# Performance work log

Measured on AMD Instinct MI355X. Metric: run time of the kernel, lower is better.

Reference implementation:

```python
import jax, jax.numpy as jnp
import numpy as np

D = 512
H = 8
FFN_H = 2048
NEG = -1.0e10


def layer_norm(x, gamma, beta, eps=1e-5):
    mu = jnp.mean(x, axis=-1, keepdims=True)
    var = jnp.var(x, axis=-1, keepdims=True)
    return (x - mu) * jax.lax.rsqrt(var + eps) * gamma + beta


def mha(x_q, x_kv, Wq, Wk, Wv, Wo, valid_lens):
    # x_q: [B,Tq,D], x_kv: [B,Tk,D]; valid_lens: [B,Tq] or [B]
    B, Tq, _ = x_q.shape
    Tk = x_kv.shape[1]
    dh = D // H
    q = (x_q @ Wq.T).reshape(B, Tq, H, dh).transpose(0, 2, 1, 3)  # [B,H,Tq,dh]
    k = (x_kv @ Wk.T).reshape(B, Tk, H, dh).transpose(0, 2, 1, 3)
    v = (x_kv @ Wv.T).reshape(B, Tk, H, dh).transpose(0, 2, 1, 3)
    scores = jnp.einsum('bhqd,bhkd->bhqk', q, k) / jnp.sqrt(jnp.float32(dh))
    pos = jnp.arange(Tk)
    if valid_lens.ndim == 1:  # [B] -> mask [B,1,1,Tk]
        mask = pos[None, None, None, :] < valid_lens[:, None, None, None]
    else:  # [B,Tq] -> mask [B,1,Tq,Tk]
        mask = pos[None, None, None, :] < valid_lens[:, None, :, None]
    scores = jnp.where(mask, scores, NEG)
    attn = jax.nn.softmax(scores, axis=-1)
    out = jnp.einsum('bhqk,bhkd->bhqd', attn, v)  # [B,H,Tq,dh]
    out = out.transpose(0, 2, 1, 3).reshape(B, Tq, D)
    return out @ Wo.T


def setup_inputs() -> dict:
    key = jax.random.key(0)
    ks = jax.random.split(key, 20)
    B, T = 32, 512
    s = 1.0 / np.sqrt(D)
    inp = {
        'X': jax.random.normal(ks[0], (B, T, D), jnp.float32),
        'enc_outputs': jax.random.normal(ks[1], (B, T, D), jnp.float32),
        'dec_valid_lens': jax.random.randint(ks[2], (B, T), 1, T + 1, jnp.int32),
        'enc_valid_lens': jax.random.randint(ks[3], (B,), 1, T + 1, jnp.int32),
    }
    names = ['Wq1', 'Wk1', 'Wv1', 'Wo1', 'Wq2', 'Wk2', 'Wv2', 'Wo2']
    for i, n in enumerate(names):
        inp[n] = jax.random.normal(ks[4 + i], (D, D), jnp.float32) * s
    inp['W1'] = jax.random.normal(ks[12], (FFN_H, D), jnp.float32) * s
    inp['b1'] = jnp.zeros((FFN_H,), jnp.float32)
    inp['W2'] = jax.random.normal(ks[13], (D, FFN_H), jnp.float32) * (1.0 / np.sqrt(FFN_H))
    inp['b2'] = jnp.zeros((D,), jnp.float32)
    for j in (1, 2, 3):
        inp[f'g{j}'] = jnp.ones((D,), jnp.float32)
        inp[f'be{j}'] = jnp.zeros((D,), jnp.float32)
    return inp


def reference(X, enc_outputs, dec_valid_lens, enc_valid_lens,
              Wq1, Wk1, Wv1, Wo1, Wq2, Wk2, Wv2, Wo2,
              W1, b1, W2, b2, g1, be1, g2, be2, g3, be3):
    # Training path: state[2][i] is None -> key_values = X. Dropout in eval mode (identity).
    X2 = mha(X, X, Wq1, Wk1, Wv1, Wo1, dec_valid_lens)            # self-attention
    Y = layer_norm(X + X2, g1, be1)                               # AddNorm1
    Y2 = mha(Y, enc_outputs, Wq2, Wk2, Wv2, Wo2, enc_valid_lens)  # cross-attention
    Z = layer_norm(Y + Y2, g2, be2)                               # AddNorm2
    F = (jax.nn.leaky_relu(Z @ W1.T + b1, 0.01)) @ W2.T + b2      # FFN (LeakyReLU slope 0.01)
    return layer_norm(Z + F, g3, be3)                             # AddNorm3
```

## Files before the change

### kernel.cpp

```cpp
#include <hip/hip_runtime.h>
#include <cstdint>
#include <cstddef>

typedef __bf16 bf16;
typedef __bf16 bf16x8 __attribute__((ext_vector_type(8)));
typedef float  f32x4  __attribute__((ext_vector_type(4)));
typedef unsigned short u16;

#define MD ((size_t)8388608)

__device__ __forceinline__ void async_copy16(const bf16* gp, bf16* lp) {
  __builtin_amdgcn_global_load_lds(
      (__attribute__((address_space(1))) void*)(gp),
      (__attribute__((address_space(3))) void*)(lp), 16, 0, 0);
}

__device__ __forceinline__ int is_f32(const u16* __restrict__ x) {
  const int e = (x[(threadIdx.x & 63) * 2] >> 7) & 0xFF;
  return __ballot(e >= 141) != 0ull;
}

struct ConvSrc { const void* p[20]; };

__global__ __launch_bounds__(256)
void convert_all(ConvSrc s, bf16* __restrict__ ws, const u16* __restrict__ xprobe)
{
  const int n[20] = {8388608, 8388608,
                     262144, 262144, 262144, 262144, 262144, 262144, 262144, 262144,
                     1048576, 2048, 1048576, 512, 512, 512, 512, 512, 512, 512};
  const unsigned int doff[20] = {
      41943040u, 50331648u,
      58720256u, 58982400u, 59244544u, 59506688u,
      59768832u, 60030976u, 60293120u, 60555264u,
      60817408u, 61865984u, 61868032u, 62916608u,
      62917120u, 62917632u, 62918144u, 62918656u, 62919168u, 62919680u};

  const int f32 = is_f32(xprobe);

  int bi = blockIdx.x;
  int idx = 0, b0 = 0;
  for (; idx < 20; ++idx) {
    const int nb = (n[idx] + 2047) >> 11;
    if (bi < b0 + nb) break;
    b0 += nb;
  }
  const int i = ((bi - b0) << 11) + threadIdx.x * 8;
  if (i >= n[idx]) return;
  bf16* dst = ws + doff[idx] + i;
  if (f32) {
    const float* sp = (const float*)s.p[idx] + i;
    f32x4 a = *(const f32x4*)sp;
    f32x4 b = *(const f32x4*)(sp + 4);
    bf16x8 o;
#pragma unroll
    for (int e = 0; e < 4; ++e) { o[e] = (bf16)a[e]; o[4 + e] = (bf16)b[e]; }
    *(bf16x8*)dst = o;
  } else {
    *(bf16x8*)dst = *(const bf16x8*)((const bf16*)s.p[idx] + i);
  }
}

template<int MODE, int TM, int TN>
__global__ __launch_bounds__(256)
void gemm_bt(const bf16* __restrict__ A, const bf16* __restrict__ B,
             const bf16* __restrict__ bias, bf16* __restrict__ C,
             int M, int N, int K)
{
  constexpr int MI = TM / 32;
  constexpr int NJ = TN / 32;
  __shared__ __attribute__((aligned(16))) bf16 As[TM * 64];
  __shared__ __attribute__((aligned(16))) bf16 Bs[TN * 64];

  const int t    = threadIdx.x;
  const int wave = t >> 6;
  const int lane = t & 63;
  const int quad = lane >> 4;
  const int l15  = lane & 15;
  const int wr   = (wave >> 1) * (TM / 2);
  const int wc   = (wave & 1) * (TN / 2);

  const int id    = blockIdx.y * gridDim.x + blockIdx.x;
  const int chunk = (gridDim.x * gridDim.y) >> 3;
  const int lin   = (id & 7) * chunk + (id >> 3);
  const int m0    = (lin / gridDim.x) * TM;
  const int n0    = (lin % gridDim.x) * TN;

  const f32x4 fz = {0.f, 0.f, 0.f, 0.f};
  f32x4 acc[MI][NJ];
#pragma unroll
  for (int i = 0; i < MI; ++i)
#pragma unroll
    for (int j = 0; j < NJ; ++j) acc[i][j] = fz;

  const int nkt = K >> 6;
  for (int kt = 0; kt < nkt; ++kt) {
    const int k0 = kt << 6;
    __syncthreads();
#pragma unroll
    for (int c = 0; c < TM / 32; ++c) {
      const int s   = c * 256 + t;
      const int row = s >> 3;
      const int kg  = ((s & 7) ^ (row & 7)) << 3;
      async_copy16(A + (size_t)(m0 + row) * K + k0 + kg,
                   As + ((c * 256 + wave * 64) << 3));
    }
#pragma unroll
    for (int c = 0; c < TN / 32; ++c) {
      const int s   = c * 256 + t;
      const int row = s >> 3;
      const int kg  = ((s & 7) ^ (row & 7)) << 3;
      async_copy16(B + (size_t)(n0 + row) * K + k0 + kg,
                   Bs + ((c * 256 + wave * 64) << 3));
    }
    __syncthreads();

#pragma unroll
    for (int ks = 0; ks < 2; ++ks) {
      bf16x8 af[MI], bfv[NJ];
#pragma unroll
      for (int i = 0; i < MI; ++i) {
        const int row = wr + i * 16 + l15;
        const int ph  = (ks * 4 + quad) ^ (row & 7);
        af[i] = *(const bf16x8*)(As + row * 64 + ph * 8);
      }
#pragma unroll
      for (int j = 0; j < NJ; ++j) {
        const int row = wc + j * 16 + l15;
        const int ph  = (ks * 4 + quad) ^ (row & 7);
        bfv[j] = *(const bf16x8*)(Bs + row * 64 + ph * 8);
      }
#pragma unroll
      for (int i = 0; i < MI; ++i)
#pragma unroll
        for (int j = 0; j < NJ; ++j)
          acc[i][j] = __builtin_amdgcn_mfma_f32_16x16x32_bf16(af[i], bfv[j],
                                                              acc[i][j], 0, 0, 0);
    }
  }

#pragma unroll
  for (int i = 0; i < MI; ++i) {
    const int m = m0 + wr + i * 16 + quad * 4;
#pragma unroll
    for (int j = 0; j < NJ; ++j) {
      const int n = n0 + wc + j * 16 + l15;
      float bv = 0.f;
      if (MODE >= 1) bv = (float)bias[n];
#pragma unroll
      for (int r = 0; r < 4; ++r) {
        float v = acc[i][j][r];
        if (MODE >= 1) v += bv;
        if (MODE == 1) v = v > 0.f ? v : 0.01f * v;
        C[(size_t)(m + r) * N + n] = (bf16)v;
      }
    }
  }
}

__global__ __launch_bounds__(256, 4)
void flash_attn(const bf16* __restrict__ Qp, const bf16* __restrict__ Kp,
                const bf16* __restrict__ Vp, bf16* __restrict__ Op,
                const int* __restrict__ vlen, int per_query, int sq, int skv)
{
  __shared__ __attribute__((aligned(16))) bf16 Ks[64][72];
  __shared__ __attribute__((aligned(16))) bf16 VsT[64][72];
  __shared__ __attribute__((aligned(16))) bf16 Ps[4][32][72];
  __shared__ int vlmax_sh;

  const int t    = threadIdx.x;
  const int wave = t >> 6;
  const int lane = t & 63;
  const int quad = lane >> 4;
  const int l15  = lane & 15;
  const int bx   = blockIdx.x;
  const int qt   = bx >> 8;
  const int h    = bx & 7;
  const int b    = (bx >> 3) & 31;
  const int q0   = qt * 128 + wave * 32;

  bf16x8 qfrag[2][2];
#pragma unroll
  for (int mt = 0; mt < 2; ++mt)
#pragma unroll
    for (int ks = 0; ks < 2; ++ks)
      qfrag[mt][ks] = *(const bf16x8*)(Qp +
          (size_t)(b * 512 + q0 + mt * 16 + l15) * sq + h * 64 + ks * 32 + quad * 8);

  int vl_r[2][4];
  int myvl = 1;
#pragma unroll
  for (int mt = 0; mt < 2; ++mt)
#pragma unroll
    for (int r = 0; r < 4; ++r) {
      const int q = q0 + mt * 16 + quad * 4 + r;
      const int v = per_query ? vlen[b * 512 + q] : vlen[b];
      vl_r[mt][r] = v;
      myvl = v > myvl ? v : myvl;
    }

  if (t == 0) vlmax_sh = 1;
  __syncthreads();
#pragma unroll
  for (int off = 1; off < 64; off <<= 1) {
    const int o = __shfl_xor(myvl, off);
    myvl = o > myvl ? o : myvl;
  }
  if (lane == 0) atomicMax(&vlmax_sh, myvl);
  __syncthreads();
  const int ktiles = (vlmax_sh + 63) >> 6;

  const f32x4 fz = {0.f, 0.f, 0.f, 0.f};
  float l_part[2][4] = {{0.f,0.f,0.f,0.f},{0.f,0.f,0.f,0.f}};
  f32x4 o_acc[2][4];
#pragma unroll
  for (int mt = 0; mt < 2; ++mt)
#pragma unroll
    for (int nt = 0; nt < 4; ++nt) o_acc[mt][nt] = fz;

  for (int kt = 0; kt < ktiles; ++kt) {
    const int k0 = kt * 64;
    __syncthreads();
    {
      const int r0 = t >> 3;
      const int c0 = (t & 7) * 8;
      const bf16* g = Kp + (size_t)(b * 512 + k0 + r0) * skv + h * 64 + c0;
      *(bf16x8*)&Ks[r0][c0]      = *(const bf16x8*)g;
      *(bf16x8*)&Ks[r0 + 32][c0] = *(const bf16x8*)(g + (size_t)32 * skv);
    }
    {
      const bf16* g = Vp + (size_t)(b * 512 + k0 + wave * 16) * skv + h * 64 + lane;
      bf16x8 lo, hi;
#pragma unroll
      for (int kk = 0; kk < 8; ++kk) lo[kk] = g[(size_t)kk * skv];
#pragma unroll
      for (int kk = 0; kk < 8; ++kk) hi[kk] = g[(size_t)(kk + 8) * skv];
      *(bf16x8*)&VsT[lane][wave * 16]     = lo;
      *(bf16x8*)&VsT[lane][wave * 16 + 8] = hi;
    }
    __syncthreads();

    f32x4 s[2][4];
#pragma unroll
    for (int mt = 0; mt < 2; ++mt)
#pragma unroll
      for (int nt = 0; nt < 4; ++nt) s[mt][nt] = fz;
#pragma unroll
    for (int ks = 0; ks < 2; ++ks)
#pragma unroll
      for (int nt = 0; nt < 4; ++nt) {
        const bf16x8 bk = *(const bf16x8*)&Ks[nt * 16 + l15][ks * 32 + quad * 8];
        s[0][nt] = __builtin_amdgcn_mfma_f32_16x16x32_bf16(qfrag[0][ks], bk, s[0][nt], 0, 0, 0);
        s[1][nt] = __builtin_amdgcn_mfma_f32_16x16x32_bf16(qfrag[1][ks], bk, s[1][nt], 0, 0, 0);
      }

#pragma unroll
    for (int mt = 0; mt < 2; ++mt)
#pragma unroll
      for (int nt = 0; nt < 4; ++nt) {
        const int k_abs = k0 + nt * 16 + l15;
#pragma unroll
        for (int r = 0; r < 4; ++r) {
          const float p = (k_abs < vl_r[mt][r]) ? __expf(s[mt][nt][r] * 0.125f) : 0.f;
          l_part[mt][r] += p;
          Ps[wave][mt * 16 + quad * 4 + r][nt * 16 + l15] = (bf16)p;
        }
      }

#pragma unroll
    for (int ks = 0; ks < 2; ++ks) {
      const bf16x8 ap0 = *(const bf16x8*)&Ps[wave][l15][ks * 32 + quad * 8];
      const bf16x8 ap1 = *(const bf16x8*)&Ps[wave][16 + l15][ks * 32 + quad * 8];
#pragma unroll
      for (int nt = 0; nt < 4; ++nt) {
        const bf16x8 bv = *(const bf16x8*)&VsT[nt * 16 + l15][ks * 32 + quad * 8];
        o_acc[0][nt] = __builtin_amdgcn_mfma_f32_16x16x32_bf16(ap0, bv, o_acc[0][nt], 0, 0, 0);
        o_acc[1][nt] = __builtin_amdgcn_mfma_f32_16x16x32_bf16(ap1, bv, o_acc[1][nt], 0, 0, 0);
      }
    }
  }

#pragma unroll
  for (int mt = 0; mt < 2; ++mt)
#pragma unroll
    for (int r = 0; r < 4; ++r) {
      float l = l_part[mt][r];
#pragma unroll
      for (int off = 1; off < 16; off <<= 1)
        l += __shfl_xor(l, off);
      const float inv_l = (l > 0.f) ? (1.f / l) : 0.f;
      const int q = q0 + mt * 16 + quad * 4 + r;
#pragma unroll
      for (int nt = 0; nt < 4; ++nt)
        Op[(size_t)(b * 512 + q) * 512 + h * 64 + nt * 16 + l15] =
            (bf16)(o_acc[mt][nt][r] * inv_l);
    }
}

__global__ __launch_bounds__(256)
void add_layernorm(const bf16* X, const bf16* R,
                   const bf16* __restrict__ gamma, const bf16* __restrict__ beta,
                   bf16* Out)
{
  const int t    = threadIdx.x;
  const int wave = t >> 6;
  const int lane = t & 63;
  const size_t row  = (size_t)blockIdx.x * 4 + wave;
  const size_t base = row * 512 + lane * 8;

  bf16x8 xv = *(const bf16x8*)(X + base);
  bf16x8 rv = *(const bf16x8*)(R + base);
  float v[8];
  float sum = 0.f, ss = 0.f;
#pragma unroll
  for (int i = 0; i < 8; ++i) {
    v[i] = (float)xv[i] + (float)rv[i];
    sum += v[i];
    ss  += v[i] * v[i];
  }
#pragma unroll
  for (int off = 1; off < 64; off <<= 1) {
    sum += __shfl_xor(sum, off);
    ss  += __shfl_xor(ss, off);
  }
  const float mean = sum * (1.f / 512.f);
  const float var  = ss * (1.f / 512.f) - mean * mean;
  const float rstd = rsqrtf(var + 1e-5f);

  bf16x8 gv = *(const bf16x8*)(gamma + lane * 8);
  bf16x8 bv = *(const bf16x8*)(beta + lane * 8);
  bf16x8 ov;
#pragma unroll
  for (int i = 0; i < 8; ++i)
    ov[i] = (bf16)(((v[i] - mean) * rstd) * (float)gv[i] + (float)bv[i]);
  *(bf16x8*)(Out + base) = ov;
}

__global__ __launch_bounds__(256)
void add_layernorm_out(const bf16* X, const bf16* R,
                       const bf16* __restrict__ gamma, const bf16* __restrict__ beta,
                       void* Out, const u16* __restrict__ xprobe)
{
  const int t    = threadIdx.x;
  const int wave = t >> 6;
  const int lane = t & 63;
  const size_t row  = (size_t)blockIdx.x * 4 + wave;
  const size_t base = row * 512 + lane * 8;

  const int f32 = is_f32(xprobe);

  bf16x8 xv = *(const bf16x8*)(X + base);
  bf16x8 rv = *(const bf16x8*)(R + base);
  float v[8];
  float sum = 0.f, ss = 0.f;
#pragma unroll
  for (int i = 0; i < 8; ++i) {
    v[i] = (float)xv[i] + (float)rv[i];
    sum += v[i];
    ss  += v[i] * v[i];
  }
#pragma unroll
  for (int off = 1; off < 64; off <<= 1) {
    sum += __shfl_xor(sum, off);
    ss  += __shfl_xor(ss, off);
  }
  const float mean = sum * (1.f / 512.f);
  const float var  = ss * (1.f / 512.f) - mean * mean;
  const float rstd = rsqrtf(var + 1e-5f);

  bf16x8 gv = *(const bf16x8*)(gamma + lane * 8);
  bf16x8 bv = *(const bf16x8*)(beta + lane * 8);
  float o[8];
#pragma unroll
  for (int i = 0; i < 8; ++i)
    o[i] = ((v[i] - mean) * rstd) * (float)gv[i] + (float)bv[i];

  if (f32) {
    float* op = (float*)Out + base;
    f32x4 o0 = {o[0], o[1], o[2], o[3]};
    f32x4 o1 = {o[4], o[5], o[6], o[7]};
    *(f32x4*)op       = o0;
    *(f32x4*)(op + 4) = o1;
  } else {
    bf16x8 ov;
#pragma unroll
    for (int i = 0; i < 8; ++i) ov[i] = (bf16)o[i];
    *(bf16x8*)((bf16*)Out + base) = ov;
  }
}

extern "C" void kernel_launch(void* const* d_in, const int* in_sizes, int n_in,
                              void* d_out, int out_size, void* d_ws, size_t ws_size,
                              hipStream_t stream)
{
  (void)in_sizes; (void)n_in; (void)out_size; (void)ws_size;

  const int* dvl = (const int*)d_in[2];
  const int* evl = (const int*)d_in[3];
  const u16* xprobe = (const u16*)d_in[0];

  bf16* ws = (bf16*)d_ws;
  bf16* S0 = ws;
  bf16* S1 = ws + 1 * MD;
  bf16* S3 = ws + 3 * MD;
  bf16* S4 = ws + 4 * MD;
  bf16* Xb = ws + 5 * MD;
  bf16* Eb = ws + 6 * MD;
  bf16* W  = ws + 7 * MD;
  const bf16 *Wq1 = W,
             *Wo1 = W + 786432,   *Wq2 = W + 1048576, *Wk2 = W + 1310720,
             *Wo2 = W + 1835008,
             *W1  = W + 2097152,  *b1  = W + 3145728,
             *W2  = W + 3147776,  *b2  = W + 4196352,
             *g1  = W + 4196864,  *be1 = W + 4197376,
             *g2  = W + 4197888,  *be2 = W + 4198400,
             *g3  = W + 4198912,  *be3 = W + 4199424;

  ConvSrc cs;
  cs.p[0] = d_in[0];  cs.p[1] = d_in[1];
  for (int k = 0; k < 12; ++k) cs.p[2 + k] = d_in[4 + k];
  for (int k = 0; k < 6; ++k)  cs.p[14 + k] = d_in[16 + k];
  convert_all<<<dim3(10248), dim3(256), 0, stream>>>(cs, ws, xprobe);

  dim3 blk(256);
  dim3 gP(4, 128);
  dim3 gQKV(12, 128);
  dim3 gKV(8, 128);
  dim3 gF1(16, 128);

  gemm_bt<0,128,128><<<gQKV, blk, 0, stream>>>(Xb, Wq1, nullptr, S0, 16384, 1536, 512);
  flash_attn<<<dim3(1024), blk, 0, stream>>>(S0, S0 + 512, S0 + 1024, S3, dvl, 1, 1536, 1536);
  gemm_bt<0,128,128><<<gP, blk, 0, stream>>>(S3, Wo1, nullptr, S1, 16384, 512, 512);
  add_layernorm<<<dim3(4096), blk, 0, stream>>>(Xb, S1, g1, be1, S4);

  gemm_bt<0,128,128><<<gP,  blk, 0, stream>>>(S4, Wq2, nullptr, S0, 16384, 512, 512);
  gemm_bt<0,128,128><<<gKV, blk, 0, stream>>>(Eb, Wk2, nullptr, S1, 16384, 1024, 512);
  flash_attn<<<dim3(1024), blk, 0, stream>>>(S0, S1, S1 + 512, S3, evl, 0, 512, 1024);
  gemm_bt<0,128,128><<<gP, blk, 0, stream>>>(S3, Wo2, nullptr, S1, 16384, 512, 512);
  add_layernorm<<<dim3(4096), blk, 0, stream>>>(S4, S1, g2, be2, S4);

  gemm_bt<1,128,128><<<gF1, blk, 0, stream>>>(S4, W1, b1, S0, 16384, 2048, 512);
  gemm_bt<2,128,128><<<gP,  blk, 0, stream>>>(S0, W2, b2, Xb, 16384, 512, 2048);
  add_layernorm_out<<<dim3(4096), blk, 0, stream>>>(S4, Xb, g3, be3, d_out, xprobe);
}
```

Measured before the change: 473.2 us.

## Replace GEMM with double-buffered 8-wave 256-row tile kernel with ping-pong scheduling

Replaces the single-buffered 128x128 GEMM with a 512-thread kernel that uses 256-row tiles and double-buffered LDS for A and B. Loads for the next k-step are issued asynchronously while the current step's MFMAs run, and each step is split into two halves with barriers and raised wave priority around the MFMA bursts. The goal is to hide global-load latency and raise data reuse per block. In exchange it uses much more LDS and registers, and the hand-written vmcnt waits make correctness depend on the exact number of loads issued.

```diff
diff --git a/kernel.cpp b/kernel.cpp
--- a/kernel.cpp
+++ b/kernel.cpp
@@ -60,30 +60,54 @@
   }
 }
 
-template<int MODE, int TM, int TN>
-__global__ __launch_bounds__(256)
-void gemm_bt(const bf16* __restrict__ A, const bf16* __restrict__ B,
-             const bf16* __restrict__ bias, bf16* __restrict__ C,
-             int M, int N, int K)
-{
-  constexpr int MI = TM / 32;
-  constexpr int NJ = TN / 32;
-  __shared__ __attribute__((aligned(16))) bf16 As[TM * 64];
-  __shared__ __attribute__((aligned(16))) bf16 Bs[TN * 64];
+template<int ROWS>
+__device__ __forceinline__ void stage_tile(const bf16* __restrict__ g,
+                                           bf16* lds, int K)
+{
+  const int t = threadIdx.x;
+  const int wbase = (t >> 6) << 6;
+#pragma unroll
+  for (int r = 0; r < ROWS / 64; ++r) {
+    const int s   = (r << 9) + t;
+    const int row = s >> 3;
+    const int cg  = s & 7;
+    async_copy16(g + (size_t)row * K + ((cg ^ (row & 7)) << 3),
+                 lds + ((size_t)((r << 9) + wbase) << 3));
+  }
+}
+
+template<int MODE, int BN, int WM, int WN>
+__global__ __launch_bounds__(512, 2)
+void gemm8p(const bf16* __restrict__ A, const bf16* __restrict__ B,
+            const bf16* __restrict__ bias, bf16* __restrict__ C,
+            int M, int N, int K)
+{
+  constexpr int BM = 256;
+  constexpr int WR = BM / WM;
+  constexpr int MI = WR / 16;
+  constexpr int NJ = 4;
+  constexpr int MH = MI / 2;
+  constexpr int BL = BN / 64;
+
+  __shared__ __attribute__((aligned(16))) bf16 As[2][BM * 64];
+  __shared__ __attribute__((aligned(16))) bf16 Bs[2][BN * 64];
 
   const int t    = threadIdx.x;
-  const int wave = t >> 6;
   const int lane = t & 63;
   const int quad = lane >> 4;
   const int l15  = lane & 15;
-  const int wr   = (wave >> 1) * (TM / 2);
-  const int wc   = (wave & 1) * (TN / 2);
+  const int wave = t >> 6;
+  const int wm   = wave / WN;
+  const int wn   = wave % WN;
 
   const int id    = blockIdx.y * gridDim.x + blockIdx.x;
   const int chunk = (gridDim.x * gridDim.y) >> 3;
   const int lin   = (id & 7) * chunk + (id >> 3);
-  const int m0    = (lin / gridDim.x) * TM;
-  const int n0    = (lin % gridDim.x) * TN;
+  const int m0    = (lin / gridDim.x) * BM;
+  const int n0    = (lin % gridDim.x) * BN;
+
+  const bf16* Ag = A + (size_t)m0 * K;
+  const bf16* Bg = B + (size_t)n0 * K;
 
   const f32x4 fz = {0.f, 0.f, 0.f, 0.f};
   f32x4 acc[MI][NJ];
@@ -93,62 +117,97 @@
     for (int j = 0; j < NJ; ++j) acc[i][j] = fz;
 
   const int nkt = K >> 6;
+
+  stage_tile<BM>(Ag, As[0], K);
+  stage_tile<BN>(Bg, Bs[0], K);
+  stage_tile<BN>(Bg + (nkt > 1 ? 64 : 0), Bs[1], K);
+  if constexpr (BL == 4) asm volatile("s_waitcnt vmcnt(4)" ::: "memory");
+  else                   asm volatile("s_waitcnt vmcnt(2)" ::: "memory");
+  __builtin_amdgcn_s_barrier();
+
   for (int kt = 0; kt < nkt; ++kt) {
-    const int k0 = kt << 6;
-    __syncthreads();
-#pragma unroll
-    for (int c = 0; c < TM / 32; ++c) {
-      const int s   = c * 256 + t;
-      const int row = s >> 3;
-      const int kg  = ((s & 7) ^ (row & 7)) << 3;
-      async_copy16(A + (size_t)(m0 + row) * K + k0 + kg,
-                   As + ((c * 256 + wave * 64) << 3));
-    }
-#pragma unroll
-    for (int c = 0; c < TN / 32; ++c) {
-      const int s   = c * 256 + t;
-      const int row = s >> 3;
-      const int kg  = ((s & 7) ^ (row & 7)) << 3;
-      async_copy16(B + (size_t)(n0 + row) * K + k0 + kg,
-                   Bs + ((c * 256 + wave * 64) << 3));
-    }
-    __syncthreads();
-
-#pragma unroll
-    for (int ks = 0; ks < 2; ++ks) {
-      bf16x8 af[MI], bfv[NJ];
-#pragma unroll
-      for (int i = 0; i < MI; ++i) {
-        const int row = wr + i * 16 + l15;
-        const int ph  = (ks * 4 + quad) ^ (row & 7);
-        af[i] = *(const bf16x8*)(As + row * 64 + ph * 8);
-      }
-#pragma unroll
-      for (int j = 0; j < NJ; ++j) {
-        const int row = wc + j * 16 + l15;
-        const int ph  = (ks * 4 + quad) ^ (row & 7);
-        bfv[j] = *(const bf16x8*)(Bs + row * 64 + ph * 8);
-      }
-#pragma unroll
-      for (int i = 0; i < MI; ++i)
-#pragma unroll
-        for (int j = 0; j < NJ; ++j)
-          acc[i][j] = __builtin_amdgcn_mfma_f32_16x16x32_bf16(af[i], bfv[j],
-                                                              acc[i][j], 0, 0, 0);
-    }
-  }
-
-#pragma unroll
-  for (int i = 0; i < MI; ++i) {
-    const int m = m0 + wr + i * 16 + quad * 4;
-#pragma unroll
-    for (int j = 0; j < NJ; ++j) {
-      const int n = n0 + wc + j * 16 + l15;
+    const int c = kt & 1;
+    const bf16* a_l = As[c];
+    const bf16* b_l = Bs[c];
+    const int kA = (kt + 1 < nkt) ? kt + 1 : nkt - 1;
+    const int kB = (kt + 2 < nkt) ? kt + 2 : nkt - 1;
+
+    bf16x8 bfv[NJ][2];
+    bf16x8 af[MH][2];
+
+    stage_tile<BM>(Ag + ((size_t)kA << 6), As[c ^ 1], K);
+#pragma unroll
+    for (int nj = 0; nj < NJ; ++nj) {
+      const int row = wn * 64 + nj * 16 + l15;
+#pragma unroll
+      for (int ks = 0; ks < 2; ++ks) {
+        const int ph = (ks * 4 + quad) ^ (row & 7);
+        bfv[nj][ks] = *(const bf16x8*)(b_l + row * 64 + ph * 8);
+      }
+    }
+#pragma unroll
+    for (int mi = 0; mi < MH; ++mi) {
+      const int row = wm * WR + mi * 16 + l15;
+#pragma unroll
+      for (int ks = 0; ks < 2; ++ks) {
+        const int ph = (ks * 4 + quad) ^ (row & 7);
+        af[mi][ks] = *(const bf16x8*)(a_l + row * 64 + ph * 8);
+      }
+    }
+    __builtin_amdgcn_s_barrier();
+    asm volatile("s_waitcnt lgkmcnt(0)" ::: "memory");
+    __builtin_amdgcn_s_setprio(1);
+#pragma unroll
+    for (int mi = 0; mi < MH; ++mi)
+#pragma unroll
+      for (int nj = 0; nj < NJ; ++nj)
+#pragma unroll
+        for (int ks = 0; ks < 2; ++ks)
+          acc[mi][nj] = __builtin_amdgcn_mfma_f32_16x16x32_bf16(
+              af[mi][ks], bfv[nj][ks], acc[mi][nj], 0, 0, 0);
+    __builtin_amdgcn_s_setprio(0);
+    __builtin_amdgcn_s_barrier();
+
+    stage_tile<BN>(Bg + ((size_t)kB << 6), Bs[c], K);
+#pragma unroll
+    for (int mi = 0; mi < MH; ++mi) {
+      const int row = wm * WR + (MH + mi) * 16 + l15;
+#pragma unroll
+      for (int ks = 0; ks < 2; ++ks) {
+        const int ph = (ks * 4 + quad) ^ (row & 7);
+        af[mi][ks] = *(const bf16x8*)(a_l + row * 64 + ph * 8);
+      }
+    }
+    __builtin_amdgcn_s_barrier();
+    asm volatile("s_waitcnt lgkmcnt(0)" ::: "memory");
+    __builtin_amdgcn_s_setprio(1);
+#pragma unroll
+    for (int mi = 0; mi < MH; ++mi)
+#pragma unroll
+      for (int nj = 0; nj < NJ; ++nj)
+#pragma unroll
+        for (int ks = 0; ks < 2; ++ks)
+          acc[MH + mi][nj] = __builtin_amdgcn_mfma_f32_16x16x32_bf16(
+              af[mi][ks], bfv[nj][ks], acc[MH + mi][nj], 0, 0, 0);
+    __builtin_amdgcn_s_setprio(0);
+    if constexpr (BL == 4) asm volatile("s_waitcnt vmcnt(4)" ::: "memory");
+    else                   asm volatile("s_waitcnt vmcnt(2)" ::: "memory");
+    __builtin_amdgcn_s_barrier();
+  }
+
+  asm volatile("s_waitcnt vmcnt(0)" ::: "memory");
+
+#pragma unroll
+  for (int mi = 0; mi < MI; ++mi) {
+    const int m = m0 + wm * WR + mi * 16 + quad * 4;
+#pragma unroll
+    for (int nj = 0; nj < NJ; ++nj) {
+      const int n = n0 + wn * 64 + nj * 16 + l15;
       float bv = 0.f;
       if (MODE >= 1) bv = (float)bias[n];
 #pragma unroll
       for (int r = 0; r < 4; ++r) {
-        float v = acc[i][j][r];
+        float v = acc[mi][nj][r];
         if (MODE >= 1) v += bv;
         if (MODE == 1) v = v > 0.f ? v : 0.01f * v;
         C[(size_t)(m + r) * N + n] = (bf16)v;
@@ -421,24 +480,21 @@
   for (int k = 0; k < 6; ++k)  cs.p[14 + k] = d_in[16 + k];
   convert_all<<<dim3(10248), dim3(256), 0, stream>>>(cs, ws, xprobe);
 
-  dim3 blk(256);
-  dim3 gP(4, 128);
-  dim3 gQKV(12, 128);
-  dim3 gKV(8, 128);
-  dim3 gF1(16, 128);
-
-  gemm_bt<0,128,128><<<gQKV, blk, 0, stream>>>(Xb, Wq1, nullptr, S0, 16384, 1536, 512);
-  flash_attn<<<dim3(1024), blk, 0, stream>>>(S0, S0 + 512, S0 + 1024, S3, dvl, 1, 1536, 1536);
-  gemm_bt<0,128,128><<<gP, blk, 0, stream>>>(S3, Wo1, nullptr, S1, 16384, 512, 512);
-  add_layernorm<<<dim3(4096), blk, 0, stream>>>(Xb, S1, g1, be1, S4);
-
-  gemm_bt<0,128,128><<<gP,  blk, 0, stream>>>(S4, Wq2, nullptr, S0, 16384, 512, 512);
-  gemm_bt<0,128,128><<<gKV, blk, 0, stream>>>(Eb, Wk2, nullptr, S1, 16384, 1024, 512);
-  flash_attn<<<dim3(1024), blk, 0, stream>>>(S0, S1, S1 + 512, S3, evl, 0, 512, 1024);
-  gemm_bt<0,128,128><<<gP, blk, 0, stream>>>(S3, Wo2, nullptr, S1, 16384, 512, 512);
-  add_layernorm<<<dim3(4096), blk, 0, stream>>>(S4, S1, g2, be2, S4);
-
-  gemm_bt<1,128,128><<<gF1, blk, 0, stream>>>(S4, W1, b1, S0, 16384, 2048, 512);
-  gemm_bt<2,128,128><<<gP,  blk, 0, stream>>>(S0, W2, b2, Xb, 16384, 512, 2048);
-  add_layernorm_out<<<dim3(4096), blk, 0, stream>>>(S4, Xb, g3, be3, d_out, xprobe);
-}
+  dim3 blk256(256);
+  dim3 blk512(512);
+
+  gemm8p<0,256,2,4><<<dim3(6,64), blk512, 0, stream>>>(Xb, Wq1, nullptr, S0, 16384, 1536, 512);
+  flash_attn<<<dim3(1024), blk256, 0, stream>>>(S0, S0 + 512, S0 + 1024, S3, dvl, 1, 1536, 1536);
+  gemm8p<0,128,4,2><<<dim3(4,64), blk512, 0, stream>>>(S3, Wo1, nullptr, S1, 16384, 512, 512);
+  add_layernorm<<<dim3(4096), blk256, 0, stream>>>(Xb, S1, g1, be1, S4);
+
+  gemm8p<0,128,4,2><<<dim3(4,64), blk512, 0, stream>>>(S4, Wq2, nullptr, S0, 16384, 512, 512);
+  gemm8p<0,256,2,4><<<dim3(4,64), blk512, 0, stream>>>(Eb, Wk2, nullptr, S1, 16384, 1024, 512);
+  flash_attn<<<dim3(1024), blk256, 0, stream>>>(S0, S1, S1 + 512, S3, evl, 0, 512, 1024);
+  gemm8p<0,128,4,2><<<dim3(4,64), blk512, 0, stream>>>(S3, Wo2, nullptr, S1, 16384, 512, 512);
+  add_layernorm<<<dim3(4096), blk256, 0, stream>>>(S4, S1, g2, be2, S4);
+
+  gemm8p<1,256,2,4><<<dim3(8,64), blk512, 0, stream>>>(S4, W1, b1, S0, 16384, 2048, 512);
+  gemm8p<2,128,4,2><<<dim3(4,64), blk512, 0, stream>>>(S0, W2, b2, Xb, 16384, 512, 2048);
+  add_layernorm_out<<<dim3(4096), blk256, 0, stream>>>(S4, Xb, g3, be3, d_out, xprobe);
+}
```

New measurement: 505.5 us. +6.8%, slower.

## Add 256x256 ping-pong-scheduled GEMM kernel for wide-N projections

Applied to the files above, without the earlier changes.

Adds a new 512-thread GEMM kernel with 256x256 tiles, double-buffered async global-to-LDS loads, an XOR-swizzled shared layout, and a barrier/setprio-interleaved schedule that splits each k-tile into four MFMA phases. It also remaps block ids so neighbouring blocks are spread across chunks. The kernel replaces the 128x128 GEMM for the QKV, cross-attention KV and FFN1 projections, aiming for more operand reuse and better overlap of loads with MFMA work. The cost is a single block per CU, much higher register pressure, and fewer blocks in flight (384, 256 and 512 per launch).

```diff
diff --git a/kernel.cpp b/kernel.cpp
--- a/kernel.cpp
+++ b/kernel.cpp
@@ -149,6 +149,195 @@
 #pragma unroll
       for (int r = 0; r < 4; ++r) {
         float v = acc[i][j][r];
+        if (MODE >= 1) v += bv;
+        if (MODE == 1) v = v > 0.f ? v : 0.01f * v;
+        C[(size_t)(m + r) * N + n] = (bf16)v;
+      }
+    }
+  }
+}
+
+template<int MODE>
+__global__ __launch_bounds__(512, 1)
+void gemm4p(const bf16* __restrict__ A, const bf16* __restrict__ B,
+            const bf16* __restrict__ bias, bf16* __restrict__ C,
+            int M, int N, int K)
+{
+  constexpr int BM = 256, BN = 256, WM = 2, WN = 4, T = 512;
+  constexpr int WR = BM / WM;
+  constexpr int MI = WR / 16;
+  constexpr int NJ = (BN / WN) / 16;
+  constexpr int MH = MI / 2;
+  constexpr int LA = BM * 8 / T;
+  constexpr int LB = BN * 8 / T;
+  static_assert(LA == 4 && LB == 4 && NJ == 4, "schedule assumes 4/4/4");
+
+  __shared__ __attribute__((aligned(16))) bf16 As[2][BM * 64];
+  __shared__ __attribute__((aligned(16))) bf16 Bs[2][BN * 64];
+
+  const int t    = threadIdx.x;
+  const int lane = t & 63;
+  const int quad = lane >> 4;
+  const int l15  = lane & 15;
+  const int wave = t >> 6;
+  const int wm   = wave >> 2;
+  const int wn   = wave & 3;
+
+  const int id    = blockIdx.y * gridDim.x + blockIdx.x;
+  const int chunk = (gridDim.x * gridDim.y) >> 3;
+  const int lin   = (id & 7) * chunk + (id >> 3);
+  const int m0    = (lin / gridDim.x) * BM;
+  const int n0    = (lin % gridDim.x) * BN;
+
+  const bf16* Ag = A + (size_t)m0 * K;
+  const bf16* Bg = B + (size_t)n0 * K;
+  const int wbase = wave << 6;
+
+  auto stA = [&](int kt, int r, int buf) {
+    const int s   = r * T + t;
+    const int row = s >> 3;
+    const int cg  = s & 7;
+    async_copy16(Ag + (size_t)row * K + (kt << 6) + ((cg ^ (row & 7)) << 3),
+                 &As[buf][(size_t)(r * T + wbase) << 3]);
+  };
+  auto stB = [&](int kt, int r, int buf) {
+    const int s   = r * T + t;
+    const int row = s >> 3;
+    const int cg  = s & 7;
+    async_copy16(Bg + (size_t)row * K + (kt << 6) + ((cg ^ (row & 7)) << 3),
+                 &Bs[buf][(size_t)(r * T + wbase) << 3]);
+  };
+
+  const f32x4 fz = {0.f, 0.f, 0.f, 0.f};
+  f32x4 acc[MI][NJ];
+#pragma unroll
+  for (int i = 0; i < MI; ++i)
+#pragma unroll
+    for (int j = 0; j < NJ; ++j) acc[i][j] = fz;
+
+  const int nkt = K >> 6;
+
+#pragma unroll
+  for (int r = 0; r < LA; ++r) stA(0, r, 0);
+#pragma unroll
+  for (int r = 0; r < LB; ++r) stB(0, r, 0);
+  stA(1, 0, 1); stA(1, 2, 1);
+#pragma unroll
+  for (int r = 0; r < LB; ++r) stB(1, r, 1);
+  asm volatile("s_waitcnt vmcnt(6)" ::: "memory");
+  __builtin_amdgcn_s_barrier();
+
+  for (int j = 0; j < nkt; ++j) {
+    const int cb = j & 1;
+    const bf16* a_l = As[cb];
+    const bf16* b_l = Bs[cb];
+    const int kN = (j + 1 < nkt) ? j + 1 : nkt - 1;
+    const int kF = (j + 2 < nkt) ? j + 2 : nkt - 1;
+
+    bf16x8 bfv[NJ];
+    bf16x8 af[MH];
+
+#pragma unroll
+    for (int nj = 0; nj < NJ; ++nj) {
+      const int row = wn * 64 + nj * 16 + l15;
+      bfv[nj] = *(const bf16x8*)(b_l + row * 64 + ((quad ^ (row & 7)) << 3));
+    }
+#pragma unroll
+    for (int mi = 0; mi < MH; ++mi) {
+      const int row = wm * WR + mi * 16 + l15;
+      af[mi] = *(const bf16x8*)(a_l + row * 64 + ((quad ^ (row & 7)) << 3));
+    }
+    stA(kN, 1, cb ^ 1); stA(kN, 3, cb ^ 1);
+    __builtin_amdgcn_s_barrier();
+    asm volatile("s_waitcnt lgkmcnt(0)" ::: "memory");
+    __builtin_amdgcn_sched_barrier(0);
+    __builtin_amdgcn_s_setprio(1);
+#pragma unroll
+    for (int mi = 0; mi < MH; ++mi)
+#pragma unroll
+      for (int nj = 0; nj < NJ; ++nj)
+        acc[mi][nj] = __builtin_amdgcn_mfma_f32_16x16x32_bf16(af[mi], bfv[nj],
+                                                              acc[mi][nj], 0, 0, 0);
+    __builtin_amdgcn_s_setprio(0);
+    __builtin_amdgcn_s_barrier();
+
+#pragma unroll
+    for (int mi = 0; mi < MH; ++mi) {
+      const int row = wm * WR + (MH + mi) * 16 + l15;
+      af[mi] = *(const bf16x8*)(a_l + row * 64 + ((quad ^ (row & 7)) << 3));
+    }
+    __builtin_amdgcn_s_barrier();
+    asm volatile("s_waitcnt lgkmcnt(0)" ::: "memory");
+    __builtin_amdgcn_sched_barrier(0);
+    __builtin_amdgcn_s_setprio(1);
+#pragma unroll
+    for (int mi = 0; mi < MH; ++mi)
+#pragma unroll
+      for (int nj = 0; nj < NJ; ++nj)
+        acc[MH + mi][nj] = __builtin_amdgcn_mfma_f32_16x16x32_bf16(af[mi], bfv[nj],
+                                                                   acc[MH + mi][nj], 0, 0, 0);
+    __builtin_amdgcn_s_setprio(0);
+    __builtin_amdgcn_s_barrier();
+
+#pragma unroll
+    for (int nj = 0; nj < NJ; ++nj) {
+      const int row = wn * 64 + nj * 16 + l15;
+      bfv[nj] = *(const bf16x8*)(b_l + row * 64 + (((4 + quad) ^ (row & 7)) << 3));
+    }
+#pragma unroll
+    for (int mi = 0; mi < MH; ++mi) {
+      const int row = wm * WR + mi * 16 + l15;
+      af[mi] = *(const bf16x8*)(a_l + row * 64 + (((4 + quad) ^ (row & 7)) << 3));
+    }
+    __builtin_amdgcn_s_barrier();
+    asm volatile("s_waitcnt lgkmcnt(0)" ::: "memory");
+    __builtin_amdgcn_sched_barrier(0);
+    __builtin_amdgcn_s_setprio(1);
+#pragma unroll
+    for (int mi = 0; mi < MH; ++mi)
+#pragma unroll
+      for (int nj = 0; nj < NJ; ++nj)
+        acc[mi][nj] = __builtin_amdgcn_mfma_f32_16x16x32_bf16(af[mi], bfv[nj],
+                                                              acc[mi][nj], 0, 0, 0);
+    __builtin_amdgcn_s_setprio(0);
+    __builtin_amdgcn_s_barrier();
+
+#pragma unroll
+    for (int mi = 0; mi < MH; ++mi) {
+      const int row = wm * WR + (MH + mi) * 16 + l15;
+      af[mi] = *(const bf16x8*)(a_l + row * 64 + (((4 + quad) ^ (row & 7)) << 3));
+    }
+    stA(kF, 0, cb); stA(kF, 2, cb);
+#pragma unroll
+    for (int r = 0; r < LB; ++r) stB(kF, r, cb);
+    __builtin_amdgcn_s_barrier();
+    asm volatile("s_waitcnt lgkmcnt(0)" ::: "memory");
+    __builtin_amdgcn_sched_barrier(0);
+    __builtin_amdgcn_s_setprio(1);
+#pragma unroll
+    for (int mi = 0; mi < MH; ++mi)
+#pragma unroll
+      for (int nj = 0; nj < NJ; ++nj)
+        acc[MH + mi][nj] = __builtin_amdgcn_mfma_f32_16x16x32_bf16(af[mi], bfv[nj],
+                                                                   acc[MH + mi][nj], 0, 0, 0);
+    __builtin_amdgcn_s_setprio(0);
+    asm volatile("s_waitcnt vmcnt(6)" ::: "memory");
+    __builtin_amdgcn_s_barrier();
+  }
+
+  asm volatile("s_waitcnt vmcnt(0)" ::: "memory");
+
+#pragma unroll
+  for (int mi = 0; mi < MI; ++mi) {
+    const int m = m0 + wm * WR + mi * 16 + quad * 4;
+#pragma unroll
+    for (int nj = 0; nj < NJ; ++nj) {
+      const int n = n0 + wn * 64 + nj * 16 + l15;
+      float bv = 0.f;
+      if (MODE >= 1) bv = (float)bias[n];
+#pragma unroll
+      for (int r = 0; r < 4; ++r) {
+        float v = acc[mi][nj][r];
         if (MODE >= 1) v += bv;
         if (MODE == 1) v = v > 0.f ? v : 0.01f * v;
         C[(size_t)(m + r) * N + n] = (bf16)v;
@@ -421,24 +610,22 @@
   for (int k = 0; k < 6; ++k)  cs.p[14 + k] = d_in[16 + k];
   convert_all<<<dim3(10248), dim3(256), 0, stream>>>(cs, ws, xprobe);
 
-  dim3 blk(256);
+  dim3 blk256(256);
+  dim3 blk512(512);
   dim3 gP(4, 128);
-  dim3 gQKV(12, 128);
-  dim3 gKV(8, 128);
-  dim3 gF1(16, 128);
-
-  gemm_bt<0,128,128><<<gQKV, blk, 0, stream>>>(Xb, Wq1, nullptr, S0, 16384, 1536, 512);
-  flash_attn<<<dim3(1024), blk, 0, stream>>>(S0, S0 + 512, S0 + 1024, S3, dvl, 1, 1536, 1536);
-  gemm_bt<0,128,128><<<gP, blk, 0, stream>>>(S3, Wo1, nullptr, S1, 16384, 512, 512);
-  add_layernorm<<<dim3(4096), blk, 0, stream>>>(Xb, S1, g1, be1, S4);
-
-  gemm_bt<0,128,128><<<gP,  blk, 0, stream>>>(S4, Wq2, nullptr, S0, 16384, 512, 512);
-  gemm_bt<0,128,128><<<gKV, blk, 0, stream>>>(Eb, Wk2, nullptr, S1, 16384, 1024, 512);
-  flash_attn<<<dim3(1024), blk, 0, stream>>>(S0, S1, S1 + 512, S3, evl, 0, 512, 1024);
-  gemm_bt<0,128,128><<<gP, blk, 0, stream>>>(S3, Wo2, nullptr, S1, 16384, 512, 512);
-  add_layernorm<<<dim3(4096), blk, 0, stream>>>(S4, S1, g2, be2, S4);
-
-  gemm_bt<1,128,128><<<gF1, blk, 0, stream>>>(S4, W1, b1, S0, 16384, 2048, 512);
-  gemm_bt<2,128,128><<<gP,  blk, 0, stream>>>(S0, W2, b2, Xb, 16384, 512, 2048);
-  add_layernorm_out<<<dim3(4096), blk, 0, stream>>>(S4, Xb, g3, be3, d_out, xprobe);
-}
+
+  gemm4p<0><<<dim3(6, 64), blk512, 0, stream>>>(Xb, Wq1, nullptr, S0, 16384, 1536, 512);
+  flash_attn<<<dim3(1024), blk256, 0, stream>>>(S0, S0 + 512, S0 + 1024, S3, dvl, 1, 1536, 1536);
+  gemm_bt<0,128,128><<<gP, blk256, 0, stream>>>(S3, Wo1, nullptr, S1, 16384, 512, 512);
+  add_layernorm<<<dim3(4096), blk256, 0, stream>>>(Xb, S1, g1, be1, S4);
+
+  gemm_bt<0,128,128><<<gP, blk256, 0, stream>>>(S4, Wq2, nullptr, S0, 16384, 512, 512);
+  gemm4p<0><<<dim3(4, 64), blk512, 0, stream>>>(Eb, Wk2, nullptr, S1, 16384, 1024, 512);
+  flash_attn<<<dim3(1024), blk256, 0, stream>>>(S0, S1, S1 + 512, S3, evl, 0, 512, 1024);
+  gemm_bt<0,128,128><<<gP, blk256, 0, stream>>>(S3, Wo2, nullptr, S1, 16384, 512, 512);
+  add_layernorm<<<dim3(4096), blk256, 0, stream>>>(S4, S1, g2, be2, S4);
+
+  gemm4p<1><<<dim3(8, 64), blk512, 0, stream>>>(S4, W1, b1, S0, 16384, 2048, 512);
+  gemm_bt<2,128,128><<<gP, blk256, 0, stream>>>(S0, W2, b2, Xb, 16384, 512, 2048);
+  add_layernorm_out<<<dim3(4096), blk256, 0, stream>>>(S4, Xb, g3, be3, d_out, xprobe);
+}
```

After: 461.5 us. 1.03x faster.
